# Optimization experiments

Measured on AMD Instinct MI355X. Metric: run time of the kernel, lower is better.

The kernel has to match this reference:

```python
import jax, jax.numpy as jnp
import numpy as np

N_POOL, DIM_EMB, DIM_HID, FIRST_DIM = 4, 128, 128, 134
N_NODES_TOT, N_GRAPHS = 250000, 256
EPS = 1e-16  # PyG softmax eps


def setup_inputs() -> dict:
    key = jax.random.key(0)
    ks = jax.random.split(key, 20)
    inp = {
        "x": jax.random.normal(ks[0], (N_NODES_TOT, FIRST_DIM), jnp.float32),
        "batch": jnp.sort(jax.random.randint(ks[1], (N_NODES_TOT,), 0, N_GRAPHS)),
        "n_nodes": jax.random.uniform(ks[2], (N_GRAPHS, 1), jnp.float32),
        "Omegas": jax.random.uniform(ks[3], (N_GRAPHS, 1), jnp.float32),
        "Phis": jax.random.uniform(ks[4], (N_GRAPHS, 1), jnp.float32),
        "Lambdas": jax.random.uniform(ks[5], (N_GRAPHS, 1), jnp.float32),
        "Omegas_norm": jax.random.uniform(ks[6], (N_GRAPHS, 1), jnp.float32),
        "Phis_norm": jax.random.uniform(ks[7], (N_GRAPHS, 1), jnp.float32),
        "Lambdas_norm": jax.random.uniform(ks[8], (N_GRAPHS, 1), jnp.float32),
    }
    s1 = 1.0 / np.sqrt(FIRST_DIM)
    s2 = 1.0 / np.sqrt(DIM_HID)
    # stacked params for the n_pool GlobalAttention modules
    inp["gate_w1"] = jax.random.uniform(ks[9], (N_POOL, FIRST_DIM, DIM_HID), jnp.float32, -s1, s1)
    inp["gate_b1"] = jax.random.uniform(ks[10], (N_POOL, DIM_HID), jnp.float32, -s1, s1)
    inp["gate_w2"] = jax.random.uniform(ks[11], (N_POOL, DIM_HID), jnp.float32, -s2, s2)
    inp["gate_b2"] = jax.random.uniform(ks[12], (N_POOL,), jnp.float32, -s2, s2)
    inp["nn_w1"] = jax.random.uniform(ks[13], (N_POOL, FIRST_DIM, DIM_HID), jnp.float32, -s1, s1)
    inp["nn_b1"] = jax.random.uniform(ks[14], (N_POOL, DIM_HID), jnp.float32, -s1, s1)
    inp["nn_w2"] = jax.random.uniform(ks[15], (N_POOL, DIM_HID, DIM_EMB), jnp.float32, -s2, s2)
    inp["nn_b2"] = jax.random.uniform(ks[16], (N_POOL, DIM_EMB), jnp.float32, -s2, s2)
    return inp


def reference(x, batch, n_nodes, Omegas, Phis, Lambdas, Omegas_norm, Phis_norm,
              Lambdas_norm, gate_w1, gate_b1, gate_w2, gate_b2, nn_w1, nn_b1,
              nn_w2, nn_b2):
    B = n_nodes.shape[0]
    # gate scores: per-node scalar per pool head -> [N, K]
    g1 = jax.nn.relu(jnp.einsum("nf,kfh->nkh", x, gate_w1) + gate_b1)
    scores = jnp.einsum("nkh,kh->nk", g1, gate_w2) + gate_b2
    # batch-segmented softmax (stable, PyG style)
    m = jax.ops.segment_max(scores, batch, num_segments=B)          # [B, K]
    e = jnp.exp(scores - m[batch])                                  # [N, K]
    denom = jax.ops.segment_sum(e, batch, num_segments=B)[batch] + EPS
    gate = e / denom                                                # [N, K]
    # node transform per pool -> [N, K, D]
    h1 = jax.nn.relu(jnp.einsum("nf,kfh->nkh", x, nn_w1) + nn_b1)
    v = jnp.einsum("nkh,khd->nkd", h1, nn_w2) + nn_b2
    # gated segment-sum pooling -> [B, K, D], concat pools -> [B, K*D]
    pooled = jax.ops.segment_sum(gate[..., None] * v, batch, num_segments=B)
    ctx_emb = pooled.reshape(B, N_POOL * DIM_EMB)
    return jnp.concatenate(
        [ctx_emb, n_nodes, Omegas, Phis, Lambdas, Omegas_norm, Phis_norm,
         Lambdas_norm], axis=1)
```

## Files before the change

### kernel.cpp

```cpp
#include <hip/hip_runtime.h>
#include <math.h>

#define N_NODES 250000
#define F_DIM   134
#define H_DIM   128
#define K_POOL  4
#define B_GR    256
#define EPSF    1e-16f
#define OUT_W   (K_POOL * H_DIM + 7)

#define BM      128
#define BK      32
#define KSTEPS  5
#define GMAX    4
#define NBLK    ((N_NODES + BM - 1) / BM)
#define TILE_USH 4096

#define SZ_XT      (NBLK * KSTEPS * TILE_USH * 2)
#define SZ_WT      (K_POOL * KSTEPS * TILE_USH * 2)
#define OFF_XH     0
#define OFF_XL     (OFF_XH + SZ_XT)
#define OFF_WHG    (OFF_XL + SZ_XT)
#define OFF_WLG    (OFF_WHG + SZ_WT)
#define OFF_WHN    (OFF_WLG + SZ_WT)
#define OFF_WLN    (OFF_WHN + SZ_WT)
#define OFF_SCORES (OFF_WLN + SZ_WT)
#define OFF_SEG    (OFF_SCORES + N_NODES * 16)
#define OFF_MAX    (OFF_SEG + 2048)
#define OFF_DEN    (OFF_MAX + 4096)
#define OFF_POOL   (OFF_DEN + 4096)

typedef __attribute__((ext_vector_type(8))) short bf16x8;
typedef __attribute__((ext_vector_type(4))) float f32x4;

__device__ __forceinline__ ushort f2bf(float f) {
    union { float f; unsigned u; } v; v.f = f;
    const unsigned u = v.u;
    return (ushort)((u + 0x7FFFu + ((u >> 16) & 1u)) >> 16);
}
__device__ __forceinline__ float bf2f(ushort h) {
    union { unsigned u; float f; } v; v.u = ((unsigned)h) << 16; return v.f;
}
__device__ __forceinline__ int swz(int row, int kg) {
    return ((row << 6) + (kg << 4)) ^ ((row & 7) << 4);
}

__device__ __forceinline__ void gld16(const ushort* g, ushort* l) {
    __builtin_amdgcn_global_load_lds(
        (const __attribute__((address_space(1))) unsigned*)g,
        (__attribute__((address_space(3))) unsigned*)l, 16, 0, 0);
}

__launch_bounds__(256)
__global__ void cvt_x_kernel(const float* __restrict__ x,
                             ushort* __restrict__ xh, ushort* __restrict__ xl)
{
    const int u = blockIdx.x * 256 + threadIdx.x;
    if (u >= NBLK * KSTEPS * 512) return;
    const int tile = u >> 9;
    const int e    = u & 511;
    const int row  = e >> 2, kg = e & 3;
    const int blk  = tile / KSTEPS, ks = tile - blk * KSTEPS;
    const int node = blk * BM + row;
    const int col0 = ks * BK + kg * 8;

    float v[8];
#pragma unroll
    for (int j = 0; j < 8; ++j) v[j] = 0.f;
    if (node < N_NODES) {
        const float* xr = x + (long)node * F_DIM + col0;
        if (col0 + 8 <= F_DIM) {
#pragma unroll
            for (int j = 0; j < 4; ++j) {
                float2 a = *(const float2*)(xr + 2 * j);
                v[2 * j] = a.x; v[2 * j + 1] = a.y;
            }
        } else if (col0 < F_DIM) {
#pragma unroll
            for (int j = 0; j < 3; ++j) {
                float2 a = *(const float2*)(xr + 2 * j);
                v[2 * j] = a.x; v[2 * j + 1] = a.y;
            }
        }
    }
    bf16x8 h, l;
#pragma unroll
    for (int j = 0; j < 8; ++j) {
        const ushort hh = f2bf(v[j]);
        h[j] = (short)hh;
        l[j] = (short)f2bf(v[j] - bf2f(hh));
    }
    const long dst = (long)tile * TILE_USH + (swz(row, kg) >> 1);
    *(bf16x8*)(xh + dst) = h;
    *(bf16x8*)(xl + dst) = l;
}

__launch_bounds__(256)
__global__ void cvt_w_kernel(const float* __restrict__ wg, const float* __restrict__ wn,
                             ushort* __restrict__ whg, ushort* __restrict__ wlg,
                             ushort* __restrict__ whn, ushort* __restrict__ wln)
{
    const int u = blockIdx.x * 256 + threadIdx.x;
    if (u >= K_POOL * KSTEPS * 512) return;
    const int tile = u >> 9;
    const int e    = u & 511;
    const int col  = e >> 2, kg = e & 3;
    const int head = tile / KSTEPS, ks = tile - head * KSTEPS;
    const int k0   = ks * BK + kg * 8;
    const float* src = blockIdx.y ? wn : wg;
    const float* sp  = src + ((long)head * F_DIM) * H_DIM + col;

    float v[8];
#pragma unroll
    for (int j = 0; j < 8; ++j)
        v[j] = (k0 + j < F_DIM) ? sp[(k0 + j) * H_DIM] : 0.f;
    bf16x8 h, l;
#pragma unroll
    for (int j = 0; j < 8; ++j) {
        const ushort hh = f2bf(v[j]);
        h[j] = (short)hh;
        l[j] = (short)f2bf(v[j] - bf2f(hh));
    }
    const long dst = (long)tile * TILE_USH + (swz(col, kg) >> 1);
    if (blockIdx.y) { *(bf16x8*)(whn + dst) = h; *(bf16x8*)(wln + dst) = l; }
    else            { *(bf16x8*)(whg + dst) = h; *(bf16x8*)(wlg + dst) = l; }
}

__device__ __forceinline__ void stage_ks(const ushort* __restrict__ Ath,
                                         const ushort* __restrict__ Atl,
                                         const ushort* __restrict__ Bth,
                                         const ushort* __restrict__ Btl,
                                         ushort* lds, int t)
{
    const int wv  = t >> 6;
    const int wo  = wv * 1024;
    const int lo8 = (t & 63) * 8;
    gld16(Ath + wo + lo8,       lds + wo);
    gld16(Ath + wo + 512 + lo8, lds + wo + 512);
    gld16(Atl + wo + lo8,       lds + 4096 + wo);
    gld16(Atl + wo + 512 + lo8, lds + 4096 + wo + 512);
    gld16(Bth + wo + lo8,       lds + 8192 + wo);
    gld16(Bth + wo + 512 + lo8, lds + 8192 + wo + 512);
    gld16(Btl + wo + lo8,       lds + 12288 + wo);
    gld16(Btl + wo + 512 + lo8, lds + 12288 + wo + 512);
}

__device__ __forceinline__ void mm_compute(int t, const ushort* Ah, const ushort* Al,
                                           const ushort* Bh, const ushort* Bl,
                                           f32x4 acc[2][8])
{
    const int lane = t & 63, wv = t >> 6;
    bf16x8 ah[2], al[2];
#pragma unroll
    for (int r = 0; r < 2; ++r) {
        const int rowA = wv * 32 + r * 16 + (lane & 15);
        const int off  = swz(rowA, lane >> 4) >> 1;
        ah[r] = *(const bf16x8*)(Ah + off);
        al[r] = *(const bf16x8*)(Al + off);
    }
#pragma unroll
    for (int c = 0; c < 8; ++c) {
        const int rowB = c * 16 + (lane & 15);
        const int off  = swz(rowB, lane >> 4) >> 1;
        const bf16x8 bh = *(const bf16x8*)(Bh + off);
        const bf16x8 bl = *(const bf16x8*)(Bl + off);
#pragma unroll
        for (int r = 0; r < 2; ++r) {
            acc[r][c] = __builtin_amdgcn_mfma_f32_16x16x32_bf16(ah[r], bh, acc[r][c], 0, 0, 0);
            acc[r][c] = __builtin_amdgcn_mfma_f32_16x16x32_bf16(ah[r], bl, acc[r][c], 0, 0, 0);
            acc[r][c] = __builtin_amdgcn_mfma_f32_16x16x32_bf16(al[r], bh, acc[r][c], 0, 0, 0);
        }
    }
}

__global__ void seg_kernel(const int* __restrict__ batch, int* __restrict__ seg) {
    int b = blockIdx.x * blockDim.x + threadIdx.x;
    if (b > B_GR) return;
    int lo = 0, hi = N_NODES;
    while (lo < hi) {
        int mid = (lo + hi) >> 1;
        if (batch[mid] < b) lo = mid + 1; else hi = mid;
    }
    seg[b] = lo;
}

__launch_bounds__(256, 2)
__global__ void gate_kernel(const ushort* __restrict__ xh, const ushort* __restrict__ xl,
                            const ushort* __restrict__ wh, const ushort* __restrict__ wl,
                            const float* __restrict__ b1,
                            const float* __restrict__ w2,
                            const float* __restrict__ b2,
                            float* __restrict__ scores)
{
    __shared__ ushort slds[16384];
    const int m0 = blockIdx.x * BM, t = threadIdx.x;
    const int lane = t & 63, wv = t >> 6;
    const ushort* Ath = xh + (long)blockIdx.x * KSTEPS * TILE_USH;
    const ushort* Atl = xl + (long)blockIdx.x * KSTEPS * TILE_USH;

    for (int k = 0; k < K_POOL; ++k) {
        const ushort* Bth = wh + (long)k * KSTEPS * TILE_USH;
        const ushort* Btl = wl + (long)k * KSTEPS * TILE_USH;

        f32x4 acc[2][8];
        const f32x4 z = {0.f, 0.f, 0.f, 0.f};
#pragma unroll
        for (int r = 0; r < 2; ++r)
#pragma unroll
            for (int c = 0; c < 8; ++c) acc[r][c] = z;

        for (int ks = 0; ks < KSTEPS; ++ks) {
            __syncthreads();
            stage_ks(Ath + ks * TILE_USH, Atl + ks * TILE_USH,
                     Bth + ks * TILE_USH, Btl + ks * TILE_USH, slds, t);
            __syncthreads();
            mm_compute(t, slds, slds + 4096, slds + 8192, slds + 12288, acc);
        }

        float b1v[8], w2v[8];
#pragma unroll
        for (int c = 0; c < 8; ++c) {
            const int col = c * 16 + (lane & 15);
            b1v[c] = b1[k * H_DIM + col];
            w2v[c] = w2[k * H_DIM + col];
        }
        const float b2v = b2[k];
#pragma unroll
        for (int r = 0; r < 2; ++r)
#pragma unroll
            for (int q = 0; q < 4; ++q) {
                float s = 0.f;
#pragma unroll
                for (int c = 0; c < 8; ++c)
                    s = fmaf(fmaxf(acc[r][c][q] + b1v[c], 0.f), w2v[c], s);
                s += __shfl_xor(s, 1); s += __shfl_xor(s, 2);
                s += __shfl_xor(s, 4); s += __shfl_xor(s, 8);
                if ((lane & 15) == 0) {
                    const int m = m0 + wv * 32 + r * 16 + (lane >> 4) * 4 + q;
                    if (m < N_NODES) scores[m * 4 + k] = s + b2v;
                }
            }
    }
}

__launch_bounds__(256)
__global__ void stats_kernel(const float* __restrict__ scores,
                             const int* __restrict__ seg,
                             float* __restrict__ maxv,
                             float* __restrict__ denom,
                             float* __restrict__ pooled)
{
    const int g = blockIdx.x;
    const int t = threadIdx.x;
    const int s = seg[g], e = seg[g + 1];
    const float4* sc4 = (const float4*)scores;

    float mx[4] = {-INFINITY, -INFINITY, -INFINITY, -INFINITY};
    for (int n = s + t; n < e; n += 256) {
        float4 v = sc4[n];
        mx[0] = fmaxf(mx[0], v.x); mx[1] = fmaxf(mx[1], v.y);
        mx[2] = fmaxf(mx[2], v.z); mx[3] = fmaxf(mx[3], v.w);
    }
#pragma unroll
    for (int c = 0; c < 4; ++c)
        for (int off = 32; off; off >>= 1)
            mx[c] = fmaxf(mx[c], __shfl_down(mx[c], off));

    __shared__ float redbuf[4][4];
    __shared__ float bmax[4];
    const int wid = t >> 6, lane = t & 63;
    if (lane == 0)
#pragma unroll
        for (int c = 0; c < 4; ++c) redbuf[wid][c] = mx[c];
    __syncthreads();
    if (t == 0)
#pragma unroll
        for (int c = 0; c < 4; ++c) {
            float m = redbuf[0][c];
            m = fmaxf(m, redbuf[1][c]); m = fmaxf(m, redbuf[2][c]); m = fmaxf(m, redbuf[3][c]);
            bmax[c] = m;
        }
    __syncthreads();
    const float m0v = bmax[0], m1v = bmax[1], m2v = bmax[2], m3v = bmax[3];

    float sm[4] = {0.f, 0.f, 0.f, 0.f};
    for (int n = s + t; n < e; n += 256) {
        float4 v = sc4[n];
        sm[0] += expf(v.x - m0v); sm[1] += expf(v.y - m1v);
        sm[2] += expf(v.z - m2v); sm[3] += expf(v.w - m3v);
    }
#pragma unroll
    for (int c = 0; c < 4; ++c)
        for (int off = 32; off; off >>= 1)
            sm[c] += __shfl_down(sm[c], off);
    __syncthreads();
    if (lane == 0)
#pragma unroll
        for (int c = 0; c < 4; ++c) redbuf[wid][c] = sm[c];
    __syncthreads();
    if (t == 0)
#pragma unroll
        for (int c = 0; c < 4; ++c) {
            maxv[g * 4 + c]  = bmax[c];
            denom[g * 4 + c] = redbuf[0][c] + redbuf[1][c] + redbuf[2][c] + redbuf[3][c] + EPSF;
        }
    pooled[g * 512 + t]       = 0.f;
    pooled[g * 512 + 256 + t] = 0.f;
}

__launch_bounds__(256, 2)
__global__ void pool_kernel(const ushort* __restrict__ xh, const ushort* __restrict__ xl,
                            const ushort* __restrict__ wh, const ushort* __restrict__ wl,
                            const int* __restrict__ batch,
                            const float* __restrict__ b1,
                            const float* __restrict__ scores,
                            const float* __restrict__ maxv,
                            const float* __restrict__ denom,
                            float* __restrict__ pooled)
{
    __shared__ ushort slds[16384];
    __shared__ float lds_pool[GMAX][K_POOL][H_DIM];
    const int m0 = blockIdx.x * BM, t = threadIdx.x;
    const int lane = t & 63, wv = t >> 6;
    const ushort* Ath = xh + (long)blockIdx.x * KSTEPS * TILE_USH;
    const ushort* Atl = xl + (long)blockIdx.x * KSTEPS * TILE_USH;

    for (int idx = t; idx < GMAX * K_POOL * H_DIM; idx += 256)
        ((float*)lds_pool)[idx] = 0.f;

    const int gfirst0 = batch[m0];

    for (int k = 0; k < K_POOL; ++k) {
        const ushort* Bth = wh + (long)k * KSTEPS * TILE_USH;
        const ushort* Btl = wl + (long)k * KSTEPS * TILE_USH;

        f32x4 acc[2][8];
        const f32x4 z = {0.f, 0.f, 0.f, 0.f};
#pragma unroll
        for (int r = 0; r < 2; ++r)
#pragma unroll
            for (int c = 0; c < 8; ++c) acc[r][c] = z;

        for (int ks = 0; ks < KSTEPS; ++ks) {
            __syncthreads();
            stage_ks(Ath + ks * TILE_USH, Atl + ks * TILE_USH,
                     Bth + ks * TILE_USH, Btl + ks * TILE_USH, slds, t);
            __syncthreads();
            mm_compute(t, slds, slds + 4096, slds + 8192, slds + 12288, acc);
        }

        float b1v[8];
#pragma unroll
        for (int c = 0; c < 8; ++c)
            b1v[c] = b1[k * H_DIM + c * 16 + (lane & 15)];

#pragma unroll
        for (int r = 0; r < 2; ++r) {
            const int mrow = m0 + wv * 32 + r * 16;
            if (mrow >= N_NODES) continue;
            const int mhi   = (mrow + 15 < N_NODES) ? mrow + 15 : N_NODES - 1;
            const int ga    = batch[mrow];
            const bool unif = (batch[mhi] == ga) && (mrow + 15 < N_NODES);
            if (unif) {
                const float mxv = maxv[ga * 4 + k];
                const float den = denom[ga * 4 + k];
                float gates[4];
#pragma unroll
                for (int q = 0; q < 4; ++q) {
                    const int m = mrow + (lane >> 4) * 4 + q;
                    gates[q] = expf(scores[m * 4 + k] - mxv) / den;
                }
                const int lg = ga - gfirst0;
#pragma unroll
                for (int c = 0; c < 8; ++c) {
                    float p = 0.f;
#pragma unroll
                    for (int q = 0; q < 4; ++q)
                        p = fmaf(gates[q], fmaxf(acc[r][c][q] + b1v[c], 0.f), p);
                    p += __shfl_xor(p, 16);
                    p += __shfl_xor(p, 32);
                    if (lane < 16) {
                        if (lg < GMAX) atomicAdd(&lds_pool[lg][k][c * 16 + lane], p);
                        else atomicAdd(&pooled[(ga * K_POOL + k) * H_DIM + c * 16 + lane], p);
                    }
                }
            } else {
#pragma unroll
                for (int q = 0; q < 4; ++q) {
                    const int m = mrow + (lane >> 4) * 4 + q;
                    const bool val = m < N_NODES;
                    int g = ga; float gate = 0.f;
                    if (val) {
                        g = batch[m];
                        gate = expf(scores[m * 4 + k] - maxv[g * 4 + k]) / denom[g * 4 + k];
                    }
                    const int lg = g - gfirst0;
#pragma unroll
                    for (int c = 0; c < 8; ++c) {
                        const float v = gate * fmaxf(acc[r][c][q] + b1v[c], 0.f);
                        if (val && v != 0.f) {
                            if (lg < GMAX) atomicAdd(&lds_pool[lg][k][c * 16 + (lane & 15)], v);
                            else atomicAdd(&pooled[(g * K_POOL + k) * H_DIM + c * 16 + (lane & 15)], v);
                        }
                    }
                }
            }
        }
    }

    __syncthreads();
    {
        const int mlast = (m0 + BM - 1 < N_NODES) ? m0 + BM - 1 : N_NODES - 1;
        int span = batch[mlast] - gfirst0 + 1;
        if (span > GMAX) span = GMAX;
        for (int idx = t; idx < span * K_POOL * H_DIM; idx += 256) {
            const float v = ((const float*)lds_pool)[idx];
            if (v != 0.f) {
                const int lg  = idx >> 9;
                const int rem = idx & 511;
                atomicAdd(&pooled[(gfirst0 + lg) * 512 + rem], v);
            }
        }
    }
}

__launch_bounds__(128)
__global__ void out_kernel(const float* __restrict__ pooled,
                           const float* __restrict__ w2,
                           const float* __restrict__ b2,
                           const float* __restrict__ denom,
                           const float* __restrict__ s0, const float* __restrict__ s1,
                           const float* __restrict__ s2, const float* __restrict__ s3,
                           const float* __restrict__ s4, const float* __restrict__ s5,
                           const float* __restrict__ s6,
                           float* __restrict__ out)
{
    const int g = blockIdx.x;
    const int t = threadIdx.x;
    __shared__ float ps[H_DIM];
    float* orow = out + g * OUT_W;

    for (int k = 0; k < K_POOL; ++k) {
        __syncthreads();
        ps[t] = pooled[(g * K_POOL + k) * H_DIM + t];
        __syncthreads();
        const float den = denom[g * 4 + k];
        const float gs  = (den - EPSF) / den;
        float a = b2[k * H_DIM + t] * gs;
        const float* wkt = w2 + (k * H_DIM) * H_DIM + t;
#pragma unroll 4
        for (int h = 0; h < H_DIM; ++h)
            a = fmaf(ps[h], wkt[h * H_DIM], a);
        orow[k * H_DIM + t] = a;
    }
    if (t < 7) {
        const float* sp;
        switch (t) {
            case 0: sp = s0; break; case 1: sp = s1; break; case 2: sp = s2; break;
            case 3: sp = s3; break; case 4: sp = s4; break; case 5: sp = s5; break;
            default: sp = s6; break;
        }
        orow[K_POOL * H_DIM + t] = sp[g];
    }
}

extern "C" void kernel_launch(void* const* d_in, const int* in_sizes, int n_in,
                              void* d_out, int out_size, void* d_ws, size_t ws_size,
                              hipStream_t stream) {
    const float* x     = (const float*)d_in[0];
    const int*   batch = (const int*)d_in[1];
    const float* n_nodes = (const float*)d_in[2];
    const float* Omegas  = (const float*)d_in[3];
    const float* Phis    = (const float*)d_in[4];
    const float* Lambdas = (const float*)d_in[5];
    const float* Omn     = (const float*)d_in[6];
    const float* Phn     = (const float*)d_in[7];
    const float* Lan     = (const float*)d_in[8];
    const float* gw1 = (const float*)d_in[9];
    const float* gb1 = (const float*)d_in[10];
    const float* gw2 = (const float*)d_in[11];
    const float* gb2 = (const float*)d_in[12];
    const float* nw1 = (const float*)d_in[13];
    const float* nb1 = (const float*)d_in[14];
    const float* nw2 = (const float*)d_in[15];
    const float* nb2 = (const float*)d_in[16];

    char* ws = (char*)d_ws;
    ushort* xh  = (ushort*)(ws + OFF_XH);
    ushort* xl  = (ushort*)(ws + OFF_XL);
    ushort* whg = (ushort*)(ws + OFF_WHG);
    ushort* wlg = (ushort*)(ws + OFF_WLG);
    ushort* whn = (ushort*)(ws + OFF_WHN);
    ushort* wln = (ushort*)(ws + OFF_WLN);
    float* scores = (float*)(ws + OFF_SCORES);
    int*   seg    = (int*)(ws + OFF_SEG);
    float* maxv   = (float*)(ws + OFF_MAX);
    float* denom  = (float*)(ws + OFF_DEN);
    float* pooled = (float*)(ws + OFF_POOL);
    float* out    = (float*)d_out;

    cvt_x_kernel<<<(NBLK * KSTEPS * 512) / 256, 256, 0, stream>>>(x, xh, xl);
    dim3 wgrid((K_POOL * KSTEPS * 512 + 255) / 256, 2);
    cvt_w_kernel<<<wgrid, 256, 0, stream>>>(gw1, nw1, whg, wlg, whn, wln);
    seg_kernel<<<2, 256, 0, stream>>>(batch, seg);

    gate_kernel<<<NBLK, 256, 0, stream>>>(xh, xl, whg, wlg, gb1, gw2, gb2, scores);
    stats_kernel<<<B_GR, 256, 0, stream>>>(scores, seg, maxv, denom, pooled);
    pool_kernel<<<NBLK, 256, 0, stream>>>(xh, xl, whn, wln, batch, nb1,
                                          scores, maxv, denom, pooled);
    out_kernel<<<B_GR, 128, 0, stream>>>(pooled, nw2, nb2, denom,
                                         n_nodes, Omegas, Phis, Lambdas, Omn, Phn, Lan, out);
}
```

Measured before the change: 623.7 us.

## Double-buffer LDS tiles to overlap global staging with MFMA compute

Flattens the per-head and k-step loops in the gate and pool kernels into one 20-step loop and double-buffers the LDS tiles. The next tile's global-to-LDS load is issued before computing on the current buffer, with one waitcnt and barrier per step instead of two syncthreads. The goal is to hide global load latency behind the matrix multiply. In exchange, LDS use doubles to 64KB per block for the staging buffers, which may reduce occupancy below the two blocks per CU requested by the launch bounds, especially in the pool kernel, which also holds lds_pool.

```diff
diff --git a/kernel.cpp b/kernel.cpp
--- a/kernel.cpp
+++ b/kernel.cpp
@@ -12,9 +12,11 @@
 #define BM      128
 #define BK      32
 #define KSTEPS  5
+#define NT      (K_POOL * KSTEPS)
 #define GMAX    4
 #define NBLK    ((N_NODES + BM - 1) / BM)
 #define TILE_USH 4096
+#define BUF_USH  16384
 
 #define SZ_XT      (NBLK * KSTEPS * TILE_USH * 2)
 #define SZ_WT      (K_POOL * KSTEPS * TILE_USH * 2)
@@ -145,10 +147,12 @@
     gld16(Btl + wo + 512 + lo8, lds + 12288 + wo + 512);
 }
 
-__device__ __forceinline__ void mm_compute(int t, const ushort* Ah, const ushort* Al,
-                                           const ushort* Bh, const ushort* Bl,
-                                           f32x4 acc[2][8])
-{
+__device__ __forceinline__ void mm_compute(int t, const ushort* buf, f32x4 acc[2][8])
+{
+    const ushort* Ah = buf;
+    const ushort* Al = buf + 4096;
+    const ushort* Bh = buf + 8192;
+    const ushort* Bl = buf + 12288;
     const int lane = t & 63, wv = t >> 6;
     bf16x8 ah[2], al[2];
 #pragma unroll
@@ -192,54 +196,69 @@
                             const float* __restrict__ b2,
                             float* __restrict__ scores)
 {
-    __shared__ ushort slds[16384];
+    __shared__ ushort slds[2 * BUF_USH];
     const int m0 = blockIdx.x * BM, t = threadIdx.x;
     const int lane = t & 63, wv = t >> 6;
     const ushort* Ath = xh + (long)blockIdx.x * KSTEPS * TILE_USH;
     const ushort* Atl = xl + (long)blockIdx.x * KSTEPS * TILE_USH;
 
-    for (int k = 0; k < K_POOL; ++k) {
-        const ushort* Bth = wh + (long)k * KSTEPS * TILE_USH;
-        const ushort* Btl = wl + (long)k * KSTEPS * TILE_USH;
-
-        f32x4 acc[2][8];
-        const f32x4 z = {0.f, 0.f, 0.f, 0.f};
-#pragma unroll
-        for (int r = 0; r < 2; ++r)
-#pragma unroll
-            for (int c = 0; c < 8; ++c) acc[r][c] = z;
-
-        for (int ks = 0; ks < KSTEPS; ++ks) {
-            __syncthreads();
-            stage_ks(Ath + ks * TILE_USH, Atl + ks * TILE_USH,
-                     Bth + ks * TILE_USH, Btl + ks * TILE_USH, slds, t);
-            __syncthreads();
-            mm_compute(t, slds, slds + 4096, slds + 8192, slds + 12288, acc);
-        }
-
-        float b1v[8], w2v[8];
-#pragma unroll
-        for (int c = 0; c < 8; ++c) {
-            const int col = c * 16 + (lane & 15);
-            b1v[c] = b1[k * H_DIM + col];
-            w2v[c] = w2[k * H_DIM + col];
-        }
-        const float b2v = b2[k];
-#pragma unroll
-        for (int r = 0; r < 2; ++r)
-#pragma unroll
-            for (int q = 0; q < 4; ++q) {
-                float s = 0.f;
-#pragma unroll
-                for (int c = 0; c < 8; ++c)
-                    s = fmaf(fmaxf(acc[r][c][q] + b1v[c], 0.f), w2v[c], s);
-                s += __shfl_xor(s, 1); s += __shfl_xor(s, 2);
-                s += __shfl_xor(s, 4); s += __shfl_xor(s, 8);
-                if ((lane & 15) == 0) {
-                    const int m = m0 + wv * 32 + r * 16 + (lane >> 4) * 4 + q;
-                    if (m < N_NODES) scores[m * 4 + k] = s + b2v;
+    f32x4 acc[2][8];
+    const f32x4 z = {0.f, 0.f, 0.f, 0.f};
+#pragma unroll
+    for (int r = 0; r < 2; ++r)
+#pragma unroll
+        for (int c = 0; c < 8; ++c) acc[r][c] = z;
+
+    stage_ks(Ath, Atl, wh, wl, slds, t);
+    asm volatile("s_waitcnt vmcnt(0)" ::: "memory");
+    __builtin_amdgcn_s_barrier();
+
+    int cur = 0;
+#pragma unroll 1
+    for (int tt = 0; tt < NT; ++tt) {
+        const int h = tt / KSTEPS, ks = tt - h * KSTEPS;
+        const int t1 = tt + 1;
+        if (t1 < NT) {
+            const int h1 = t1 / KSTEPS, ks1 = t1 - h1 * KSTEPS;
+            stage_ks(Ath + ks1 * TILE_USH, Atl + ks1 * TILE_USH,
+                     wh + ((long)h1 * KSTEPS + ks1) * TILE_USH,
+                     wl + ((long)h1 * KSTEPS + ks1) * TILE_USH,
+                     slds + (cur ^ 1) * BUF_USH, t);
+        }
+        mm_compute(t, slds + cur * BUF_USH, acc);
+
+        if (ks == KSTEPS - 1) {
+            float b1v[8], w2v[8];
+#pragma unroll
+            for (int c = 0; c < 8; ++c) {
+                const int col = c * 16 + (lane & 15);
+                b1v[c] = b1[h * H_DIM + col];
+                w2v[c] = w2[h * H_DIM + col];
+            }
+            const float b2v = b2[h];
+#pragma unroll
+            for (int r = 0; r < 2; ++r)
+#pragma unroll
+                for (int q = 0; q < 4; ++q) {
+                    float s = 0.f;
+#pragma unroll
+                    for (int c = 0; c < 8; ++c)
+                        s = fmaf(fmaxf(acc[r][c][q] + b1v[c], 0.f), w2v[c], s);
+                    s += __shfl_xor(s, 1); s += __shfl_xor(s, 2);
+                    s += __shfl_xor(s, 4); s += __shfl_xor(s, 8);
+                    if ((lane & 15) == 0) {
+                        const int m = m0 + wv * 32 + r * 16 + (lane >> 4) * 4 + q;
+                        if (m < N_NODES) scores[m * 4 + h] = s + b2v;
+                    }
                 }
-            }
+#pragma unroll
+            for (int r = 0; r < 2; ++r)
+#pragma unroll
+                for (int c = 0; c < 8; ++c) acc[r][c] = z;
+        }
+        asm volatile("s_waitcnt vmcnt(0)" ::: "memory");
+        __builtin_amdgcn_s_barrier();
+        cur ^= 1;
     }
 }
 
@@ -318,7 +337,7 @@
                             const float* __restrict__ denom,
                             float* __restrict__ pooled)
 {
-    __shared__ ushort slds[16384];
+    __shared__ ushort slds[2 * BUF_USH];
     __shared__ float lds_pool[GMAX][K_POOL][H_DIM];
     const int m0 = blockIdx.x * BM, t = threadIdx.x;
     const int lane = t & 63, wv = t >> 6;
@@ -330,82 +349,97 @@
 
     const int gfirst0 = batch[m0];
 
-    for (int k = 0; k < K_POOL; ++k) {
-        const ushort* Bth = wh + (long)k * KSTEPS * TILE_USH;
-        const ushort* Btl = wl + (long)k * KSTEPS * TILE_USH;
-
-        f32x4 acc[2][8];
-        const f32x4 z = {0.f, 0.f, 0.f, 0.f};
-#pragma unroll
-        for (int r = 0; r < 2; ++r)
-#pragma unroll
-            for (int c = 0; c < 8; ++c) acc[r][c] = z;
-
-        for (int ks = 0; ks < KSTEPS; ++ks) {
-            __syncthreads();
-            stage_ks(Ath + ks * TILE_USH, Atl + ks * TILE_USH,
-                     Bth + ks * TILE_USH, Btl + ks * TILE_USH, slds, t);
-            __syncthreads();
-            mm_compute(t, slds, slds + 4096, slds + 8192, slds + 12288, acc);
-        }
-
-        float b1v[8];
-#pragma unroll
-        for (int c = 0; c < 8; ++c)
-            b1v[c] = b1[k * H_DIM + c * 16 + (lane & 15)];
-
-#pragma unroll
-        for (int r = 0; r < 2; ++r) {
-            const int mrow = m0 + wv * 32 + r * 16;
-            if (mrow >= N_NODES) continue;
-            const int mhi   = (mrow + 15 < N_NODES) ? mrow + 15 : N_NODES - 1;
-            const int ga    = batch[mrow];
-            const bool unif = (batch[mhi] == ga) && (mrow + 15 < N_NODES);
-            if (unif) {
-                const float mxv = maxv[ga * 4 + k];
-                const float den = denom[ga * 4 + k];
-                float gates[4];
-#pragma unroll
-                for (int q = 0; q < 4; ++q) {
-                    const int m = mrow + (lane >> 4) * 4 + q;
-                    gates[q] = expf(scores[m * 4 + k] - mxv) / den;
-                }
-                const int lg = ga - gfirst0;
-#pragma unroll
-                for (int c = 0; c < 8; ++c) {
-                    float p = 0.f;
-#pragma unroll
-                    for (int q = 0; q < 4; ++q)
-                        p = fmaf(gates[q], fmaxf(acc[r][c][q] + b1v[c], 0.f), p);
-                    p += __shfl_xor(p, 16);
-                    p += __shfl_xor(p, 32);
-                    if (lane < 16) {
-                        if (lg < GMAX) atomicAdd(&lds_pool[lg][k][c * 16 + lane], p);
-                        else atomicAdd(&pooled[(ga * K_POOL + k) * H_DIM + c * 16 + lane], p);
+    f32x4 acc[2][8];
+    const f32x4 z = {0.f, 0.f, 0.f, 0.f};
+#pragma unroll
+    for (int r = 0; r < 2; ++r)
+#pragma unroll
+        for (int c = 0; c < 8; ++c) acc[r][c] = z;
+
+    stage_ks(Ath, Atl, wh, wl, slds, t);
+    asm volatile("s_waitcnt vmcnt(0)" ::: "memory");
+    __builtin_amdgcn_s_barrier();
+
+    int cur = 0;
+#pragma unroll 1
+    for (int tt = 0; tt < NT; ++tt) {
+        const int h = tt / KSTEPS, ks = tt - h * KSTEPS;
+        const int t1 = tt + 1;
+        if (t1 < NT) {
+            const int h1 = t1 / KSTEPS, ks1 = t1 - h1 * KSTEPS;
+            stage_ks(Ath + ks1 * TILE_USH, Atl + ks1 * TILE_USH,
+                     wh + ((long)h1 * KSTEPS + ks1) * TILE_USH,
+                     wl + ((long)h1 * KSTEPS + ks1) * TILE_USH,
+                     slds + (cur ^ 1) * BUF_USH, t);
+        }
+        mm_compute(t, slds + cur * BUF_USH, acc);
+
+        if (ks == KSTEPS - 1) {
+            float b1v[8];
+#pragma unroll
+            for (int c = 0; c < 8; ++c)
+                b1v[c] = b1[h * H_DIM + c * 16 + (lane & 15)];
+
+#pragma unroll
+            for (int r = 0; r < 2; ++r) {
+                const int mrow = m0 + wv * 32 + r * 16;
+                if (mrow >= N_NODES) continue;
+                const int mhi   = (mrow + 15 < N_NODES) ? mrow + 15 : N_NODES - 1;
+                const int ga    = batch[mrow];
+                const bool unif = (batch[mhi] == ga) && (mrow + 15 < N_NODES);
+                if (unif) {
+                    const float mxv = maxv[ga * 4 + h];
+                    const float den = denom[ga * 4 + h];
+                    float gates[4];
+#pragma unroll
+                    for (int q = 0; q < 4; ++q) {
+                        const int m = mrow + (lane >> 4) * 4 + q;
+                        gates[q] = expf(scores[m * 4 + h] - mxv) / den;
                     }
-                }
-            } else {
-#pragma unroll
-                for (int q = 0; q < 4; ++q) {
-                    const int m = mrow + (lane >> 4) * 4 + q;
-                    const bool val = m < N_NODES;
-                    int g = ga; float gate = 0.f;
-                    if (val) {
-                        g = batch[m];
-                        gate = expf(scores[m * 4 + k] - maxv[g * 4 + k]) / denom[g * 4 + k];
+                    const int lg = ga - gfirst0;
+#pragma unroll
+                    for (int c = 0; c < 8; ++c) {
+                        float p = 0.f;
+#pragma unroll
+                        for (int q = 0; q < 4; ++q)
+                            p = fmaf(gates[q], fmaxf(acc[r][c][q] + b1v[c], 0.f), p);
+                        p += __shfl_xor(p, 16);
+                        p += __shfl_xor(p, 32);
+                        if (lane < 16) {
+                            if (lg < GMAX) atomicAdd(&lds_pool[lg][h][c * 16 + lane], p);
+                            else atomicAdd(&pooled[(ga * K_POOL + h) * H_DIM + c * 16 + lane], p);
+                        }
                     }
-                    const int lg = g - gfirst0;
-#pragma unroll
-                    for (int c = 0; c < 8; ++c) {
-                        const float v = gate * fmaxf(acc[r][c][q] + b1v[c], 0.f);
-                        if (val && v != 0.f) {
-                            if (lg < GMAX) atomicAdd(&lds_pool[lg][k][c * 16 + (lane & 15)], v);
-                            else atomicAdd(&pooled[(g * K_POOL + k) * H_DIM + c * 16 + (lane & 15)], v);
+                } else {
+#pragma unroll
+                    for (int q = 0; q < 4; ++q) {
+                        const int m = mrow + (lane >> 4) * 4 + q;
+                        const bool val = m < N_NODES;
+                        int g = ga; float gate = 0.f;
+                        if (val) {
+                            g = batch[m];
+                            gate = expf(scores[m * 4 + h] - maxv[g * 4 + h]) / denom[g * 4 + h];
+                        }
+                        const int lg = g - gfirst0;
+#pragma unroll
+                        for (int c = 0; c < 8; ++c) {
+                            const float v = gate * fmaxf(acc[r][c][q] + b1v[c], 0.f);
+                            if (val && v != 0.f) {
+                                if (lg < GMAX) atomicAdd(&lds_pool[lg][h][c * 16 + (lane & 15)], v);
+                                else atomicAdd(&pooled[(g * K_POOL + h) * H_DIM + c * 16 + (lane & 15)], v);
+                            }
                         }
                     }
                 }
             }
-        }
+#pragma unroll
+            for (int r = 0; r < 2; ++r)
+#pragma unroll
+                for (int c = 0; c < 8; ++c) acc[r][c] = z;
+        }
+        asm volatile("s_waitcnt vmcnt(0)" ::: "memory");
+        __builtin_amdgcn_s_barrier();
+        cur ^= 1;
     }
 
     __syncthreads();
```

New measurement: 637.6 us. +2.2%, slower.
